# Optimization experiments

Measured on AMD Instinct MI355X. Metric: run time of the kernel, lower is better.

Reference implementation:

```python
import jax, jax.numpy as jnp
import numpy as np

H = 64                      # hidden_dim
LMAX = 3                    # hidden_lmax
DIMS = [2 * l + 1 for l in range(LMAX + 1)]   # [1, 3, 5, 7]
SIZES = [H * d for d in DIMS]                 # per-l block widths: [64, 192, 320, 448]
D_IN = sum(SIZES)                             # 1024
OUT_DIM = 128
N_ATOMS = 131072
B = 512

# e3nn normalize2mom constant for SiLU: (E_{z~N(0,1)}[silu(z)^2])^{-1/2} (~1.679)
_z = np.random.default_rng(0).standard_normal(1_000_000)
_s = _z / (1.0 + np.exp(-_z))
CST = np.float32(1.0 / np.sqrt(np.mean(_s * _s)))


def _silu(x):
    return CST * (x * jax.nn.sigmoid(x))


def setup_inputs() -> dict:
    key = jax.random.key(0)
    ks = jax.random.split(key, 16)
    inp = {
        "x": jax.random.normal(ks[0], (N_ATOMS, D_IN), dtype=jnp.float32),
        "batch_indices": jax.random.randint(ks[1], (N_ATOMS,), 0, B),
        "batch_size": B,
    }
    i = 2
    for layer in range(2):
        # l=0 path: H scalars -> H*(LMAX+1) scalars (scalars + gates); l>0: H -> H
        inp[f"W{layer}_0"] = jax.random.normal(ks[i], (H, H * (LMAX + 1)), dtype=jnp.float32); i += 1
        for l in range(1, LMAX + 1):
            inp[f"W{layer}_{l}"] = jax.random.normal(ks[i], (H, H), dtype=jnp.float32); i += 1
    inp["W_out"] = jax.random.normal(ks[i], (H, OUT_DIM), dtype=jnp.float32)
    return inp


def _layer(x, Ws):
    """e3nn Linear (block-diag per l, 1/sqrt(fan_in) norm) followed by Gate."""
    N = x.shape[0]
    parts = jnp.split(x, np.cumsum(SIZES)[:-1].tolist(), axis=1)
    norm = np.float32(1.0 / np.sqrt(H))
    y0 = (parts[0] @ Ws[0]) * norm  # (N, 4H): H scalars + 3H gates
    yl = [jnp.einsum('nmc,mo->noc', parts[l].reshape(N, H, DIMS[l]), Ws[l]) * norm
          for l in range(1, LMAX + 1)]
    s = _silu(y0[:, :H])            # activated scalars
    g = _silu(y0[:, H:])            # activated gates, (N, 3H)
    out = [s]
    for l in range(1, LMAX + 1):
        gl = g[:, (l - 1) * H:l * H]                 # (N, H)
        out.append((gl[:, :, None] * yl[l - 1]).reshape(N, H * DIMS[l]))
    return jnp.concatenate(out, axis=1)              # (N, D_IN)


def reference(x, batch_indices, batch_size, W0_0, W0_1, W0_2, W0_3,
              W1_0, W1_1, W1_2, W1_3, W_out):
    h = _layer(x, [W0_0, W0_1, W0_2, W0_3])
    h = _layer(h, [W1_0, W1_1, W1_2, W1_3])
    # dropout is identity in eval mode
    # output Linear to OUT_DIM x 0e: only the scalar (0e) block has a path
    out = (h[:, :H] @ W_out) * np.float32(1.0 / np.sqrt(H))  # (N, OUT_DIM)
    return jax.ops.segment_sum(out, batch_indices, num_segments=batch_size)
```

## Files before the change

### kernel.cpp

```cpp
#include <hip/hip_runtime.h>
#include <hip/hip_bf16.h>

#define CSTF 1.676543f
#define NREP 16

typedef __bf16 bf16x8 __attribute__((ext_vector_type(8)));
typedef float  f32x4  __attribute__((ext_vector_type(4)));

__device__ __forceinline__ float silu_n(float y) {
    return CSTF * y / (1.0f + __expf(-y));
}

struct XG { f32x4 a, b, c, d; };

__device__ __forceinline__ XG loadx(const float* p) {
    XG r;
    r.a = *(const f32x4*)(p);
    r.b = *(const f32x4*)(p + 4);
    r.c = *(const f32x4*)(p + 32);
    r.d = *(const f32x4*)(p + 36);
    return r;
}

__device__ __forceinline__ void cvtfrag(const XG& v, bf16x8& a0, bf16x8& a1) {
#pragma unroll
    for (int j = 0; j < 4; ++j) {
        a0[j]     = (__bf16)v.a[j];
        a0[j + 4] = (__bf16)v.b[j];
        a1[j]     = (__bf16)v.c[j];
        a1[j + 4] = (__bf16)v.d[j];
    }
}

__global__ __launch_bounds__(256, 2) void phase1(
    const float* __restrict__ x, const int* __restrict__ bidx,
    const float* __restrict__ W0, const float* __restrict__ W1,
    float* __restrict__ S)
{
    __shared__ __align__(16) __hip_bfloat16 sb[4][16][72];
    const int tid  = threadIdx.x;
    const int lane = tid & 63;
    const int w    = tid >> 6;
    const int c    = lane & 15;
    const int g    = lane >> 4;

    bf16x8 wf0[2][4], wf1[2][4];
#pragma unroll
    for (int ks = 0; ks < 2; ++ks)
#pragma unroll
        for (int nt = 0; nt < 4; ++nt) {
            bf16x8 f0, f1;
#pragma unroll
            for (int j = 0; j < 8; ++j) {
                const int k = ks * 32 + g * 8 + j;
                f0[j] = (__bf16)(0.125f * W0[k * 256 + nt * 16 + c]);
                f1[j] = (__bf16)(0.125f * W1[k * 256 + nt * 16 + c]);
            }
            wf0[ks][nt] = f0;
            wf1[ks][nt] = f1;
        }

    float* Srep = S + ((size_t)(blockIdx.x & (NREP - 1)) << 15);
    const int wbase = (blockIdx.x * 4 + w) * 64;
    const float* px = x + (size_t)(wbase + c) * 1024 + g * 8;

    XG cur = loadx(px);
#pragma unroll 1
    for (int gi = 0; gi < 4; ++gi) {
        XG nxt = cur;
        if (gi < 3) nxt = loadx(px + (size_t)(gi + 1) * 16 * 1024);
        const int gbase = wbase + gi * 16;

        bf16x8 a0, a1;
        cvtfrag(cur, a0, a1);

        const f32x4 zf = {0.f, 0.f, 0.f, 0.f};
#pragma unroll
        for (int nt = 0; nt < 4; ++nt) {
            f32x4 acc = __builtin_amdgcn_mfma_f32_16x16x32_bf16(a0, wf0[0][nt], zf, 0, 0, 0);
            acc = __builtin_amdgcn_mfma_f32_16x16x32_bf16(a1, wf0[1][nt], acc, 0, 0, 0);
#pragma unroll
            for (int r = 0; r < 4; ++r)
                sb[w][4 * g + r][nt * 16 + c] = __float2bfloat16(silu_n(acc[r]));
        }

        const bf16x8 sa0 = *(const bf16x8*)&sb[w][c][g * 8];
        const bf16x8 sa1 = *(const bf16x8*)&sb[w][c][g * 8 + 32];

        int br[4];
#pragma unroll
        for (int r = 0; r < 4; ++r) br[r] = bidx[gbase + 4 * g + r];

#pragma unroll
        for (int nt = 0; nt < 4; ++nt) {
            f32x4 z = __builtin_amdgcn_mfma_f32_16x16x32_bf16(sa0, wf1[0][nt], zf, 0, 0, 0);
            z = __builtin_amdgcn_mfma_f32_16x16x32_bf16(sa1, wf1[1][nt], z, 0, 0, 0);
#pragma unroll
            for (int r = 0; r < 4; ++r)
                atomicAdd(&Srep[(br[r] << 6) + nt * 16 + c], silu_n(z[r]));
        }
        cur = nxt;
    }
}

__global__ __launch_bounds__(128) void phase2(
    const float* __restrict__ S, const float* __restrict__ Wout,
    float* __restrict__ out)
{
    __shared__ float sp[64];
    const int b = blockIdx.x, t = threadIdx.x;
    if (t < 64) {
        float s = 0.f;
#pragma unroll
        for (int r = 0; r < NREP; ++r) s += S[((size_t)r << 15) + (b << 6) + t];
        sp[t] = s;
    }
    __syncthreads();
    float acc = 0.f;
#pragma unroll
    for (int o = 0; o < 64; ++o) acc = fmaf(sp[o], Wout[o * 128 + t], acc);
    out[b * 128 + t] = 0.125f * acc;
}

extern "C" void kernel_launch(void* const* d_in, const int* in_sizes, int n_in,
                              void* d_out, int out_size, void* d_ws, size_t ws_size,
                              hipStream_t stream)
{
    const float* x    = (const float*)d_in[0];
    const int*   bidx = (const int*)d_in[1];
    const float* W0   = (const float*)d_in[3];
    const float* W1   = (const float*)d_in[7];
    const float* Wout = (const float*)d_in[11];
    float* S   = (float*)d_ws;
    float* out = (float*)d_out;

    hipMemsetAsync(S, 0, (size_t)NREP * 32768 * sizeof(float), stream);
    hipLaunchKernelGGL(phase1, dim3(512), dim3(256), 0, stream, x, bidx, W0, W1, S);
    hipLaunchKernelGGL(phase2, dim3(512), dim3(128), 0, stream, S, Wout, out);
}
```

Before: 46.10 us.

## Halve per-wave rows, double grid, hoist loads before weight setup

Each wave now processes 32 atoms instead of 64, and the grid doubles to 1024 blocks with a launch-bounds hint for 3 blocks per CU. Both x tiles and the batch indices are loaded up front as vector loads, before the weight fragments are built, so that memory latency overlaps the weight setup. The division in silu is replaced with a hardware reciprocal. In exchange, every block repeats the weight-fragment construction, so twice as much of that overhead is paid in total, and register pressure rises from holding two x tiles at once.

Result: slower. 49.47 us (+7.3%).

```diff
diff --git a/kernel.cpp b/kernel.cpp
--- a/kernel.cpp
+++ b/kernel.cpp
@@ -8,7 +8,7 @@
 typedef float  f32x4  __attribute__((ext_vector_type(4)));
 
 __device__ __forceinline__ float silu_n(float y) {
-    return CSTF * y / (1.0f + __expf(-y));
+    return CSTF * y * __builtin_amdgcn_rcpf(1.0f + __expf(-y));
 }
 
 struct XG { f32x4 a, b, c, d; };
@@ -22,17 +22,36 @@
     return r;
 }
 
-__device__ __forceinline__ void cvtfrag(const XG& v, bf16x8& a0, bf16x8& a1) {
-#pragma unroll
-    for (int j = 0; j < 4; ++j) {
-        a0[j]     = (__bf16)v.a[j];
-        a0[j + 4] = (__bf16)v.b[j];
-        a1[j]     = (__bf16)v.c[j];
-        a1[j + 4] = (__bf16)v.d[j];
-    }
+#define PROC16(cur, vb) { \
+  bf16x8 a0, a1; \
+  _Pragma("unroll") \
+  for (int j = 0; j < 4; ++j) { \
+    a0[j] = (__bf16)cur.a[j]; a0[j+4] = (__bf16)cur.b[j]; \
+    a1[j] = (__bf16)cur.c[j]; a1[j+4] = (__bf16)cur.d[j]; \
+  } \
+  const f32x4 zf = {0.f, 0.f, 0.f, 0.f}; \
+  _Pragma("unroll") \
+  for (int nt = 0; nt < 4; ++nt) { \
+    f32x4 acc = __builtin_amdgcn_mfma_f32_16x16x32_bf16(a0, wf0[0][nt], zf, 0, 0, 0); \
+    acc = __builtin_amdgcn_mfma_f32_16x16x32_bf16(a1, wf0[1][nt], acc, 0, 0, 0); \
+    _Pragma("unroll") \
+    for (int r = 0; r < 4; ++r) \
+      sb[w][4*g + r][nt*16 + c] = __float2bfloat16(silu_n(acc[r])); \
+  } \
+  const bf16x8 sa0 = *(const bf16x8*)&sb[w][c][g*8]; \
+  const bf16x8 sa1 = *(const bf16x8*)&sb[w][c][g*8 + 32]; \
+  _Pragma("unroll") \
+  for (int nt = 0; nt < 4; ++nt) { \
+    f32x4 z = __builtin_amdgcn_mfma_f32_16x16x32_bf16(sa0, wf1[0][nt], zf, 0, 0, 0); \
+    z = __builtin_amdgcn_mfma_f32_16x16x32_bf16(sa1, wf1[1][nt], z, 0, 0, 0); \
+    atomicAdd(&Srep[(vb.x << 6) + nt*16 + c], silu_n(z[0])); \
+    atomicAdd(&Srep[(vb.y << 6) + nt*16 + c], silu_n(z[1])); \
+    atomicAdd(&Srep[(vb.z << 6) + nt*16 + c], silu_n(z[2])); \
+    atomicAdd(&Srep[(vb.w << 6) + nt*16 + c], silu_n(z[3])); \
+  } \
 }
 
-__global__ __launch_bounds__(256, 2) void phase1(
+__global__ __launch_bounds__(256, 3) void phase1(
     const float* __restrict__ x, const int* __restrict__ bidx,
     const float* __restrict__ W0, const float* __restrict__ W1,
     float* __restrict__ S)
@@ -43,6 +62,14 @@
     const int w    = tid >> 6;
     const int c    = lane & 15;
     const int g    = lane >> 4;
+
+    const int wbase = (blockIdx.x * 4 + w) * 32;
+    const float* px = x + (size_t)(wbase + c) * 1024 + g * 8;
+
+    XG c0 = loadx(px);
+    XG c1 = loadx(px + 16 * 1024);
+    const int4 vb0 = *(const int4*)&bidx[wbase + 4 * g];
+    const int4 vb1 = *(const int4*)&bidx[wbase + 16 + 4 * g];
 
     bf16x8 wf0[2][4], wf1[2][4];
 #pragma unroll
@@ -61,46 +88,9 @@
         }
 
     float* Srep = S + ((size_t)(blockIdx.x & (NREP - 1)) << 15);
-    const int wbase = (blockIdx.x * 4 + w) * 64;
-    const float* px = x + (size_t)(wbase + c) * 1024 + g * 8;
 
-    XG cur = loadx(px);
-#pragma unroll 1
-    for (int gi = 0; gi < 4; ++gi) {
-        XG nxt = cur;
-        if (gi < 3) nxt = loadx(px + (size_t)(gi + 1) * 16 * 1024);
-        const int gbase = wbase + gi * 16;
-
-        bf16x8 a0, a1;
-        cvtfrag(cur, a0, a1);
-
-        const f32x4 zf = {0.f, 0.f, 0.f, 0.f};
-#pragma unroll
-        for (int nt = 0; nt < 4; ++nt) {
-            f32x4 acc = __builtin_amdgcn_mfma_f32_16x16x32_bf16(a0, wf0[0][nt], zf, 0, 0, 0);
-            acc = __builtin_amdgcn_mfma_f32_16x16x32_bf16(a1, wf0[1][nt], acc, 0, 0, 0);
-#pragma unroll
-            for (int r = 0; r < 4; ++r)
-                sb[w][4 * g + r][nt * 16 + c] = __float2bfloat16(silu_n(acc[r]));
-        }
-
-        const bf16x8 sa0 = *(const bf16x8*)&sb[w][c][g * 8];
-        const bf16x8 sa1 = *(const bf16x8*)&sb[w][c][g * 8 + 32];
-
-        int br[4];
-#pragma unroll
-        for (int r = 0; r < 4; ++r) br[r] = bidx[gbase + 4 * g + r];
-
-#pragma unroll
-        for (int nt = 0; nt < 4; ++nt) {
-            f32x4 z = __builtin_amdgcn_mfma_f32_16x16x32_bf16(sa0, wf1[0][nt], zf, 0, 0, 0);
-            z = __builtin_amdgcn_mfma_f32_16x16x32_bf16(sa1, wf1[1][nt], z, 0, 0, 0);
-#pragma unroll
-            for (int r = 0; r < 4; ++r)
-                atomicAdd(&Srep[(br[r] << 6) + nt * 16 + c], silu_n(z[r]));
-        }
-        cur = nxt;
-    }
+    PROC16(c0, vb0);
+    PROC16(c1, vb1);
 }
 
 __global__ __launch_bounds__(128) void phase2(
@@ -135,6 +125,6 @@
     float* out = (float*)d_out;
 
     hipMemsetAsync(S, 0, (size_t)NREP * 32768 * sizeof(float), stream);
-    hipLaunchKernelGGL(phase1, dim3(512), dim3(256), 0, stream, x, bidx, W0, W1, S);
+    hipLaunchKernelGGL(phase1, dim3(1024), dim3(256), 0, stream, x, bidx, W0, W1, S);
     hipLaunchKernelGGL(phase2, dim3(512), dim3(128), 0, stream, S, Wout, out);
 }
```
